# Performance work log

Hardware: AMD Instinct MI355X
Metric: run time of the kernel (lower is better)

The kernel has to match this reference:

```python
import jax, jax.numpy as jnp
import numpy as np

N_NODES = 49
FEAT_DIM = 1280            # efficientnet_v2_s feature dim
NODE_DIM = FEAT_DIM // N_NODES  # 26
GAT_HID = 256
HEADS = 4
NUM_CLASSES = 5
BATCH = 8192


def _grid_edges():
    # 7x7 grid, 8-neighborhood, as in _create_grid_edges, plus PyG default self loops
    edges = []
    for i in range(7):
        for j in range(7):
            node = i * 7 + j
            for di in (-1, 0, 1):
                for dj in (-1, 0, 1):
                    if di == 0 and dj == 0:
                        continue
                    ni, nj = i + di, j + dj
                    if 0 <= ni < 7 and 0 <= nj < 7:
                        edges.append((node, ni * 7 + nj))
    edges += [(n, n) for n in range(N_NODES)]  # add_self_loops=True (PyG default)
    return np.asarray(edges, dtype=np.int64).T  # [2, 361]


def setup_inputs() -> dict:
    key = jax.random.key(0)
    ks = jax.random.split(key, 16)
    s = 0.05
    inp = {
        "x": jax.random.normal(ks[0], (BATCH, FEAT_DIM), jnp.float32),
        "transform_w": jax.random.normal(ks[1], (FEAT_DIM, N_NODES * NODE_DIM), jnp.float32) * s,
        "transform_b": jnp.zeros((N_NODES * NODE_DIM,), jnp.float32),
        # GATv2 layer 1: 26 -> 64 per head, 4 heads, concat -> 256
        "g1_wl": jax.random.normal(ks[2], (NODE_DIM, GAT_HID), jnp.float32) * s,
        "g1_wr": jax.random.normal(ks[3], (NODE_DIM, GAT_HID), jnp.float32) * s,
        "g1_att": jax.random.normal(ks[4], (HEADS, GAT_HID // HEADS), jnp.float32) * s,
        "g1_b": jnp.zeros((GAT_HID,), jnp.float32),
        # GATv2 layer 2: 256 -> 256, 1 head, mean
        "g2_wl": jax.random.normal(ks[5], (GAT_HID, GAT_HID), jnp.float32) * s,
        "g2_wr": jax.random.normal(ks[6], (GAT_HID, GAT_HID), jnp.float32) * s,
        "g2_att": jax.random.normal(ks[7], (1, GAT_HID), jnp.float32) * s,
        "g2_b": jnp.zeros((GAT_HID,), jnp.float32),
        "fc_w": jax.random.normal(ks[8], (NODE_DIM + GAT_HID, NUM_CLASSES), jnp.float32) * s,
        "fc_b": jnp.zeros((NUM_CLASSES,), jnp.float32),
        "edge_index": jnp.asarray(_grid_edges()),
    }
    return inp


def _gatv2(x, src, dst, wl, wr, att, b, heads, out_ch, concat):
    # PyG GATv2Conv (share_weights=False, negative_slope=0.2, eval mode)
    n = x.shape[0]
    xl = (x @ wl).reshape(n, heads, out_ch)  # source messages
    xr = (x @ wr).reshape(n, heads, out_ch)  # target side of attention
    e = jax.nn.leaky_relu(xl[src] + xr[dst], 0.2)        # [E, H, C]
    score = jnp.einsum('ehc,hc->eh', e, att)             # [E, H]
    smax = jax.ops.segment_max(score, dst, num_segments=n)
    ex = jnp.exp(score - smax[dst])
    den = jax.ops.segment_sum(ex, dst, num_segments=n)
    alpha = ex / den[dst]                                # softmax over in-edges per node
    out = jax.ops.segment_sum(xl[src] * alpha[..., None], dst, num_segments=n)  # [N,H,C]
    out = out.reshape(n, heads * out_ch) if concat else out.mean(axis=1)
    return out + b


def reference(x, transform_w, transform_b, g1_wl, g1_wr, g1_att, g1_b,
              g2_wl, g2_wr, g2_att, g2_b, fc_w, fc_b, edge_index):
    src, dst = edge_index[0], edge_index[1]
    node = (x @ transform_w + transform_b).reshape(-1, N_NODES, NODE_DIM)  # [B,49,26]

    def graph(nf):
        h = _gatv2(nf, src, dst, g1_wl, g1_wr, g1_att, g1_b, HEADS, GAT_HID // HEADS, True)
        h = jax.nn.elu(h)  # dropout inactive in eval
        h = _gatv2(h, src, dst, g2_wl, g2_wr, g2_att, g2_b, 1, GAT_HID, False)
        return h  # [49, 256]

    g = jax.vmap(graph)(node)                              # [B,49,256]
    pooled = jnp.concatenate([node, g], axis=-1).mean(axis=1)  # [B, 282]
    return pooled @ fc_w + fc_b
```

## Files before the change

kernel.cpp:

```cpp
#include <hip/hip_runtime.h>
#include <hip/hip_bf16.h>

typedef __bf16 bf16;
typedef __attribute__((ext_vector_type(8))) __bf16 bf16x8;
typedef __attribute__((ext_vector_type(4))) __bf16 bf16x4;
typedef __attribute__((ext_vector_type(4))) float f32x4;

constexpr int BATCH = 8192, NN = 49, ND = 26, NOUT = 1274, FD = 1280;
constexpr int HID = 256, NE = 361, HEADS = 4;
constexpr int KT_X = 40;
constexpr int MT_X = 512;
constexpr int NB_W = 10;
constexpr int NTB  = 9;

constexpr size_t OFF_XPACK = 0;
constexpr size_t SZ_XPACK  = (size_t)MT_X * KT_X * 512 * 2;
constexpr size_t OFF_WPACK = OFF_XPACK + SZ_XPACK;
constexpr size_t SZ_WPACK  = (size_t)NB_W * NTB * KT_X * 512 * 2;
constexpr size_t OFF_B1    = OFF_WPACK + SZ_WPACK;
constexpr size_t SZ_B1     = (size_t)32 * 512 * 2;
constexpr size_t OFF_B2    = OFF_B1 + SZ_B1;
constexpr size_t SZ_B2     = (size_t)32 * 8 * 512 * 2;
constexpr size_t OFF_N32   = OFF_B2 + SZ_B2;
constexpr size_t SZ_N32    = (size_t)BATCH * NN * 32 * 2;
constexpr size_t OFF_PN    = OFF_N32 + SZ_N32;
constexpr size_t SZ_PN     = (size_t)BATCH * ND * 4;
constexpr size_t OFF_CSR   = OFF_PN + SZ_PN;
constexpr size_t SZ_CSR    = 8192;
constexpr size_t OFF_CHUNK = OFF_CSR + SZ_CSR;


__global__ __launch_bounds__(256) void k_pack_x(const float* __restrict__ x,
                                                bf16* __restrict__ xp) {
    int g = blockIdx.x * 256 + threadIdx.x;
    int lane = g & 63, frag = g >> 6;
    int mt = frag / KT_X, kt = frag - mt * KT_X;
    int row = mt * 16 + (lane & 15);
    int k0  = kt * 32 + (lane >> 4) * 8;
    const float* src = x + (size_t)row * FD + k0;
    bf16x8 v;
#pragma unroll
    for (int j = 0; j < 8; ++j) v[j] = (bf16)src[j];
    *(bf16x8*)(xp + ((size_t)frag * 64 + lane) * 8) = v;
}

__global__ __launch_bounds__(256) void k_pack_w(const float* __restrict__ w,
                                                bf16* __restrict__ wp) {
    int g = blockIdx.x * 256 + threadIdx.x;
    int lane = g & 63, frag = g >> 6;
    int kt = frag % KT_X, t2 = frag / KT_X;
    int nt = t2 % NTB, nb = t2 / NTB;
    int col = nb * 130 + nt * 16 + (lane & 15);
    int k0  = kt * 32 + (lane >> 4) * 8;
    bool ok = (col < NOUT) && (col < nb * 130 + 130);
    bf16x8 v;
#pragma unroll
    for (int j = 0; j < 8; ++j)
        v[j] = ok ? (bf16)w[(size_t)(k0 + j) * NOUT + col] : (bf16)0.f;
    *(bf16x8*)(wp + ((size_t)frag * 64 + lane) * 8) = v;
}

__global__ __launch_bounds__(256) void k_pack_g1(const float* __restrict__ wl,
                                                 const float* __restrict__ wr,
                                                 bf16* __restrict__ bp) {
    int g = blockIdx.x * 256 + threadIdx.x;
    int lane = g & 63, nt = g >> 6;
    int n  = nt * 16 + (lane & 15);
    int k0 = (lane >> 4) * 8;
    bf16x8 v;
#pragma unroll
    for (int j = 0; j < 8; ++j) {
        int k = k0 + j;
        float f = 0.f;
        if (k < ND) f = (n < HID) ? wl[k * HID + n] : wr[k * HID + (n - HID)];
        v[j] = (bf16)f;
    }
    *(bf16x8*)(bp + ((size_t)nt * 64 + lane) * 8) = v;
}

__global__ __launch_bounds__(256) void k_pack_g2(const float* __restrict__ wl,
                                                 const float* __restrict__ wr,
                                                 bf16* __restrict__ bp) {
    int g = blockIdx.x * 256 + threadIdx.x;
    int lane = g & 63, frag = g >> 6;
    int nt = frag >> 3, kt = frag & 7;
    int n  = nt * 16 + (lane & 15);
    int k0 = kt * 32 + (lane >> 4) * 8;
    bf16x8 v;
#pragma unroll
    for (int j = 0; j < 8; ++j) {
        int k = k0 + j;
        float f = (n < HID) ? wl[k * HID + n] : wr[k * HID + (n - HID)];
        v[j] = (bf16)f;
    }
    *(bf16x8*)(bp + ((size_t)frag * 64 + lane) * 8) = v;
}

__global__ __launch_bounds__(128) void k_csr_par(const int* __restrict__ ei,
                                                 int* __restrict__ csr) {
    __shared__ int es[NE], ed[NE], cnt[NN], ocnt[NN], off[NN + 1], ooff[NN + 1];
    int tid = threadIdx.x;
    if (tid < NN) { cnt[tid] = 0; ocnt[tid] = 0; }
    for (int e = tid; e < NE; e += 128) { es[e] = ei[e]; ed[e] = ei[NE + e]; }
    __syncthreads();
    for (int e = tid; e < NE; e += 128) {
        atomicAdd(&cnt[ed[e]], 1);
        atomicAdd(&ocnt[es[e]], 1);
    }
    __syncthreads();
    if (tid == 0) {
        off[0] = 0; ooff[0] = 0;
        for (int n = 0; n < NN; ++n) {
            off[n + 1] = off[n] + cnt[n];
            ooff[n + 1] = ooff[n] + ocnt[n];
        }
    }
    __syncthreads();
    if (tid < NN) {
        int p = off[tid];
        for (int e = 0; e < NE; ++e)
            if (ed[e] == tid) { csr[50 + p] = e; csr[411 + p] = es[e]; ++p; }
    } else if (tid >= 64 && tid < 64 + NN) {
        int n = tid - 64;
        int p = ooff[n];
        for (int e = 0; e < NE; ++e)
            if (es[e] == n) { csr[822 + p] = e; ++p; }
    }
    if (tid < 50) { csr[tid] = off[tid]; csr[772 + tid] = ooff[tid]; }
}

__global__ __launch_bounds__(256, 2) void k_gemm_node(const bf16* __restrict__ xp,
                                                      const bf16* __restrict__ wp,
                                                      const float* __restrict__ tb,
                                                      bf16* __restrict__ node32) {
    __shared__ bf16 L[128][148];
    __shared__ float tbS[144];
    int tid = threadIdx.x, lane = tid & 63, w = tid >> 6;
    int nb = blockIdx.y, C0 = nb * 130;
    int mt0 = blockIdx.x * 16 + w * 4;
    if (tid < 144) { int col = C0 + tid; tbS[tid] = (col < NOUT) ? tb[col] : 0.f; }
    f32x4 acc[4][9] = {};
    const bf16* wpB = wp + (size_t)(nb * NTB) * KT_X * 512;
    for (int kt = 0; kt < KT_X; ++kt) {
        bf16x8 a[4];
#pragma unroll
        for (int i = 0; i < 4; ++i)
            a[i] = *(const bf16x8*)(xp + (((size_t)(mt0 + i) * KT_X + kt) * 64 + lane) * 8);
#pragma unroll
        for (int j = 0; j < NTB; ++j) {
            bf16x8 b = *(const bf16x8*)(wpB + ((size_t)(j * KT_X + kt) * 64 + lane) * 8);
#pragma unroll
            for (int i = 0; i < 4; ++i)
                acc[i][j] = __builtin_amdgcn_mfma_f32_16x16x32_bf16(a[i], b, acc[i][j], 0, 0, 0);
        }
    }
    int c0 = lane & 15, r0 = (lane >> 4) * 4;
    int nodes = (nb == 9) ? 4 : 5;
    int total = 128 * nodes * 4;
    for (int half = 0; half < 2; ++half) {
        __syncthreads();
        if ((w >> 1) == half) {
            int lrbase = (w & 1) * 64;
#pragma unroll
            for (int i = 0; i < 4; ++i) {
#pragma unroll
                for (int j = 0; j < NTB; ++j) {
                    int col = j * 16 + c0;
                    float bias = tbS[col];
#pragma unroll
                    for (int r = 0; r < 4; ++r)
                        L[lrbase + i * 16 + r0 + r][col] = (bf16)(acc[i][j][r] + bias);
                }
            }
        }
        __syncthreads();
        int B0 = blockIdx.x * 256 + half * 128;
        for (int t = tid; t < total; t += 256) {
            int q = t & 3, t2 = t >> 2;
            int n_l = t2 % nodes, brow = t2 / nodes;
            bf16x8 o;
#pragma unroll
            for (int jj = 0; jj < 8; ++jj) {
                int d = q * 8 + jj;
                o[jj] = (d < ND) ? L[brow][n_l * 26 + d] : (bf16)0.f;
            }
            *(bf16x8*)(node32 + (((size_t)(B0 + brow) * NN + nb * 5 + n_l) * 32 + q * 8)) = o;
        }
    }
}

__global__ __launch_bounds__(256) void k_pool(const bf16* __restrict__ node32,
                                              float* __restrict__ pN) {
    int b = blockIdx.x * 8 + (threadIdx.x >> 5);
    int d = threadIdx.x & 31;
    if (d >= ND) return;
    const bf16* base = node32 + (size_t)b * NN * 32 + d;
    float s = 0.f;
    for (int n = 0; n < NN; ++n) s += (float)base[n * 32];
    pN[b * ND + d] = s;
}

__global__ __launch_bounds__(512, 2) void k_fuse1(const bf16* __restrict__ n32,
                                                  const bf16* __restrict__ B1p,
                                                  bf16* __restrict__ h1f,
                                                  const float* __restrict__ att1,
                                                  const float* __restrict__ g1b,
                                                  const int* __restrict__ ei,
                                                  const int* __restrict__ csr) {
    __shared__ __align__(16) char X[NN * 1024];
    __shared__ __align__(16) float attS[256];
    __shared__ float sc[NE * 4], srden[NN * 4], bS[256];
    __shared__ int ieOff[50], ieId[NE], ieSrc[NE], srcS[NE], dstS[NE];

    int tid = threadIdx.x, lane = tid & 63, w = tid >> 6, g = blockIdx.x;

    for (int i = tid; i < 256; i += 512) { attS[i] = att1[i]; bS[i] = g1b[i]; }
    for (int i = tid; i < NE; i += 512) {
        srcS[i] = ei[i]; dstS[i] = ei[NE + i];
        ieId[i] = csr[50 + i]; ieSrc[i] = csr[411 + i];
    }
    if (tid < 50) ieOff[tid] = csr[tid];

    {
        int mt = w & 3, ng = w >> 2;
        int m = mt * 16 + (lane & 15);
        bf16x8 bfrag = {};
        if (m < NN)
            bfrag = *(const bf16x8*)(n32 + ((size_t)(g * NN + m) * 32 + (lane >> 4) * 8));
        int chq = (lane >> 4) * 4;
        int sw = (m & 7) << 4;
        char* rowp = X + m * 1024;
#pragma unroll
        for (int j = 0; j < 16; ++j) {
            f32x4 z = {0.f, 0.f, 0.f, 0.f};
            bf16x8 afrag = *(const bf16x8*)(B1p + ((size_t)(ng * 16 + j) * 64 + lane) * 8);
            f32x4 acc = __builtin_amdgcn_mfma_f32_16x16x32_bf16(afrag, bfrag, z, 0, 0, 0);
            if (m < NN) {
                int ch = (ng * 16 + j) * 16 + chq;
                bf16x4 o4;
#pragma unroll
                for (int r = 0; r < 4; ++r) o4[r] = (bf16)acc[r];
                *(bf16x4*)(rowp + ((ch * 2) ^ sw)) = o4;
            }
        }
    }
    __syncthreads();

    int rot = tid & 7;
    for (int task = tid; task < NE * 4; task += 512) {
        int h = task / NE, e = task - h * NE;
        int s = srcS[e], d = dstS[e];
        int sws = (s & 7) << 4, swd = (d & 7) << 4;
        const char* ps = X + s * 1024;
        const char* pd = X + d * 1024;
        float pa[4] = {0.f, 0.f, 0.f, 0.f};
#pragma unroll
        for (int i = 0; i < 8; ++i) {
            int cc = ((i + rot) & 7) * 8;
            bf16x8 xl = *(const bf16x8*)(ps + (((h * 64 + cc) * 2) ^ sws));
            bf16x8 xr = *(const bf16x8*)(pd + (((256 + h * 64 + cc) * 2) ^ swd));
            float4 a0 = *(const float4*)(attS + h * 64 + cc);
            float4 a1 = *(const float4*)(attS + h * 64 + cc + 4);
            const float aa[8] = {a0.x, a0.y, a0.z, a0.w, a1.x, a1.y, a1.z, a1.w};
#pragma unroll
            for (int q = 0; q < 8; ++q) {
                float v = (float)xl[q] + (float)xr[q];
                v = v > 0.f ? v : 0.2f * v;
                pa[q & 3] = fmaf(aa[q], v, pa[q & 3]);
            }
        }
        sc[e * 4 + h] = (pa[0] + pa[1]) + (pa[2] + pa[3]);
    }
    __syncthreads();
    for (int t = tid; t < NN * 4; t += 512) {
        int n = t >> 2, h = t & 3;
        float m = -1e30f;
        for (int j = ieOff[n]; j < ieOff[n + 1]; ++j) m = fmaxf(m, sc[ieId[j] * 4 + h]);
        float den = 0.f;
        for (int j = ieOff[n]; j < ieOff[n + 1]; ++j) {
            int idx = ieId[j] * 4 + h;
            float ex = __expf(sc[idx] - m);
            sc[idx] = ex; den += ex;
        }
        srden[t] = 1.f / den;
    }
    __syncthreads();
    for (int task = tid; task < NN * 32; task += 512) {
        int n = task >> 5, cb = task & 31;
        int ch0 = cb * 8, hh = cb >> 3;
        float a8[8] = {};
        int j0 = ieOff[n], j1 = ieOff[n + 1];
        for (int j = j0; j < j1; ++j) {
            float al = sc[ieId[j] * 4 + hh];
            int s = ieSrc[j];
            bf16x8 xv = *(const bf16x8*)(X + s * 1024 + ((ch0 * 2) ^ ((s & 7) << 4)));
#pragma unroll
            for (int q = 0; q < 8; ++q) a8[q] = fmaf(al, (float)xv[q], a8[q]);
        }
        float rs = srden[n * 4 + hh];
        bf16x8 o;
#pragma unroll
        for (int q = 0; q < 8; ++q) {
            float v = fmaf(a8[q], rs, bS[ch0 + q]);
            v = v > 0.f ? v : (__expf(v) - 1.f);
            o[q] = (bf16)v;
        }
        int Rl = g * NN + n;
        int kt = ch0 >> 5, kg = (ch0 >> 3) & 3;
        size_t addr = (((size_t)(Rl >> 4) * 8 + kt) * 64 + (Rl & 15) + 16 * kg) * 8;
        *(bf16x8*)(h1f + addr) = o;
    }
}

__global__ __launch_bounds__(256) void k_gemm_l2(const bf16* __restrict__ Af,
                                                 const bf16* __restrict__ Bf,
                                                 bf16* __restrict__ xlr) {
    __shared__ bf16 LT[128][136];
    int tid = threadIdx.x, lane = tid & 63, w = tid >> 6;
    int mtb = blockIdx.x * 8 + (w >> 1) * 4;
    int ntb = blockIdx.y * 8 + (w & 1) * 4;
    f32x4 acc[4][4] = {};
    for (int kt = 0; kt < 8; ++kt) {
        bf16x8 a[4], b[4];
#pragma unroll
        for (int i = 0; i < 4; ++i)
            a[i] = *(const bf16x8*)(Af + (((size_t)(mtb + i) * 8 + kt) * 64 + lane) * 8);
#pragma unroll
        for (int j = 0; j < 4; ++j)
            b[j] = *(const bf16x8*)(Bf + (((size_t)(ntb + j) * 8 + kt) * 64 + lane) * 8);
#pragma unroll
        for (int i = 0; i < 4; ++i)
#pragma unroll
            for (int j = 0; j < 4; ++j)
                acc[i][j] = __builtin_amdgcn_mfma_f32_16x16x32_bf16(a[i], b[j], acc[i][j], 0, 0, 0);
    }
    int c0 = lane & 15, r0 = (lane >> 4) * 4;
    int lr0 = (w >> 1) * 64, lc0 = (w & 1) * 64;
#pragma unroll
    for (int i = 0; i < 4; ++i)
#pragma unroll
        for (int j = 0; j < 4; ++j)
#pragma unroll
            for (int r = 0; r < 4; ++r)
                LT[lr0 + i * 16 + r0 + r][lc0 + j * 16 + c0] = (bf16)acc[i][j][r];
    __syncthreads();
    size_t R0 = (size_t)blockIdx.x * 128, C0 = (size_t)blockIdx.y * 128;
#pragma unroll
    for (int it = 0; it < 8; ++it) {
        int idx = (it * 256 + tid) * 8;
        int r = idx >> 7, c = idx & 127;
        bf16x8 v = *(const bf16x8*)&LT[r][c];
        *(bf16x8*)(xlr + (R0 + r) * 512 + C0 + c) = v;
    }
}

static __device__ __forceinline__ float waveReduceSum(float v) {
#pragma unroll
    for (int m = 32; m > 0; m >>= 1) v += __shfl_xor(v, m, 64);
    return v;
}

__global__ __launch_bounds__(384, 2) void k_post2(const bf16* __restrict__ xlr,
                                                  const float* __restrict__ att2,
                                                  const float* __restrict__ pN,
                                                  const float* __restrict__ g2b,
                                                  const float* __restrict__ fcw,
                                                  const float* __restrict__ fcb,
                                                  const int* __restrict__ ei,
                                                  const int* __restrict__ csr,
                                                  int graph_base,
                                                  float* __restrict__ out) {
    __shared__ __align__(16) char X[NN * 1024];
    __shared__ float attS[256];
    __shared__ float sc[NE], sm[NN], sr[NN], wS[NN];
    __shared__ float poolS[288];
    int tid = threadIdx.x, g = blockIdx.x;
    const char* srcp = (const char*)(xlr + (size_t)g * NN * 512);
    for (int off = tid * 16; off < NN * 1024; off += 384 * 16) {
        int row = off >> 10;
        *(uint4*)(X + (off ^ ((row & 7) << 4))) = *(const uint4*)(srcp + off);
    }
    if (tid < 256) attS[tid] = att2[tid];
    if (tid >= 256 && tid < 256 + ND)
        poolS[tid - 256] = pN[(size_t)(graph_base + g) * ND + (tid - 256)] * (1.f / NN);
    __syncthreads();
    if (tid < NE) {
        int s = ei[tid], d = ei[NE + tid];
        int sws = (s & 7) << 4, swd = (d & 7) << 4;
        const char* ps = X + s * 1024;
        const char* pd = X + d * 1024;
        int rot = tid & 7;
        float pa[4] = {0.f, 0.f, 0.f, 0.f};
#pragma unroll 8
        for (int i = 0; i < 32; ++i) {
            int cc = ((i + rot) & 31) * 8;
            bf16x8 xl = *(const bf16x8*)(ps + ((cc * 2) ^ sws));
            bf16x8 xr = *(const bf16x8*)(pd + (((256 + cc) * 2) ^ swd));
            float4 a0 = *(const float4*)(attS + cc);
            float4 a1 = *(const float4*)(attS + cc + 4);
            const float aa[8] = {a0.x, a0.y, a0.z, a0.w, a1.x, a1.y, a1.z, a1.w};
#pragma unroll
            for (int q = 0; q < 8; ++q) {
                float v = (float)xl[q] + (float)xr[q];
                v = v > 0.f ? v : 0.2f * v;
                pa[q & 3] = fmaf(aa[q], v, pa[q & 3]);
            }
        }
        sc[tid] = (pa[0] + pa[1]) + (pa[2] + pa[3]);
    }
    __syncthreads();
    if (tid < NN) {
        int j0 = csr[tid], j1 = csr[tid + 1];
        float m = -1e30f;
        for (int j = j0; j < j1; ++j) m = fmaxf(m, sc[csr[50 + j]]);
        float den = 0.f;
        for (int j = j0; j < j1; ++j) den += __expf(sc[csr[50 + j]] - m);
        sm[tid] = m; sr[tid] = 1.f / den;
    }
    __syncthreads();
    if (tid < NN) {
        float wa = 0.f;
        int j0 = csr[772 + tid], j1 = csr[772 + tid + 1];
        for (int j = j0; j < j1; ++j) {
            int e = csr[822 + j];
            int d = ei[NE + e];
            wa += __expf(sc[e] - sm[d]) * sr[d];
        }
        wS[tid] = wa;
    }
    __syncthreads();
    if (tid < HID) {
        float acc = 0.f;
#pragma unroll
        for (int n = 0; n < NN; ++n) {
            float v = (float)*(const bf16*)(X + n * 1024 + ((tid * 2) ^ ((n & 7) << 4)));
            acc = fmaf(wS[n], v, acc);
        }
        poolS[ND + tid] = acc * (1.f / NN) + g2b[tid];
    }
    __syncthreads();
    int w5 = tid >> 6, lane = tid & 63;
    if (w5 < 5) {
        float a = 0.f;
        for (int d = lane; d < ND + HID; d += 64) a = fmaf(poolS[d], fcw[d * 5 + w5], a);
        a = waveReduceSum(a);
        if (lane == 0) out[(size_t)(graph_base + g) * 5 + w5] = a + fcb[w5];
    }
}

extern "C" void kernel_launch(void* const* d_in, const int* in_sizes, int n_in,
                              void* d_out, int out_size, void* d_ws, size_t ws_size,
                              hipStream_t stream) {
    const float* x   = (const float*)d_in[0];
    const float* tw  = (const float*)d_in[1];
    const float* tb  = (const float*)d_in[2];
    const float* wl1 = (const float*)d_in[3];
    const float* wr1 = (const float*)d_in[4];
    const float* at1 = (const float*)d_in[5];
    const float* b1  = (const float*)d_in[6];
    const float* wl2 = (const float*)d_in[7];
    const float* wr2 = (const float*)d_in[8];
    const float* at2 = (const float*)d_in[9];
    const float* b2  = (const float*)d_in[10];
    const float* fcw = (const float*)d_in[11];
    const float* fcb = (const float*)d_in[12];
    const int*   ei  = (const int*)d_in[13];
    float* out = (float*)d_out;

    char* ws = (char*)d_ws;
    bf16*  xp   = (bf16*)(ws + OFF_XPACK);
    bf16*  wp   = (bf16*)(ws + OFF_WPACK);
    bf16*  b1p  = (bf16*)(ws + OFF_B1);
    bf16*  b2p  = (bf16*)(ws + OFF_B2);
    bf16*  n32  = (bf16*)(ws + OFF_N32);
    float* pN   = (float*)(ws + OFF_PN);
    int*   csr  = (int*)(ws + OFF_CSR);

    const size_t perC = 50176 + 12544;
    int C = 512;
    for (int cand : {2048, 1024, 512}) {
        if (OFF_CHUNK + (size_t)cand * perC <= ws_size) { C = cand; break; }
    }
    bf16*  xlr = (bf16*)(ws + OFF_CHUNK);
    bf16*  h1f = (bf16*)(ws + OFF_CHUNK + (size_t)C * 50176);
    int nchunks = BATCH / C;
    int MtC = C * NN / 16;

    k_pack_x<<<dim3(MT_X * KT_X * 64 / 256), dim3(256), 0, stream>>>(x, xp);
    k_pack_w<<<dim3(NB_W * NTB * KT_X * 64 / 256), dim3(256), 0, stream>>>(tw, wp);
    k_pack_g1<<<dim3(8), dim3(256), 0, stream>>>(wl1, wr1, b1p);
    k_pack_g2<<<dim3(64), dim3(256), 0, stream>>>(wl2, wr2, b2p);
    k_csr_par<<<dim3(1), dim3(128), 0, stream>>>(ei, csr);
    k_gemm_node<<<dim3(32, NB_W), dim3(256), 0, stream>>>(xp, wp, tb, n32);
    k_pool<<<dim3(BATCH / 8), dim3(256), 0, stream>>>(n32, pN);

    for (int c = 0; c < nchunks; ++c) {
        const bf16* n32c = n32 + (size_t)c * C * NN * 32;
        k_fuse1<<<dim3(C), dim3(512), 0, stream>>>(n32c, b1p, h1f, at1, b1, ei, csr);
        k_gemm_l2<<<dim3(MtC / 8, 4), dim3(256), 0, stream>>>(h1f, b2p, xlr);
        k_post2<<<dim3(C), dim3(384), 0, stream>>>(xlr, at2, pN, b2, fcw, fcb,
                                                   ei, csr, c * C, out);
    }
}
```

Baseline: 959.2 us.

## Fuse layer-2 GEMM into per-graph attention kernel, dropping xlr round trip

Removes the separate layer-2 GEMM kernel and computes each graph's xl/xr projection inside the post-processing kernel with MFMA, writing results straight into swizzled shared memory. h1f is repacked per graph (padded to 64 rows) so each block reads its own A tiles, which eliminates the global xlr buffer write and reread and one launch per chunk. In exchange, each block rereads the full 256x512 B matrix from cache, pads 49 rows to 64, and holds 128 accumulator vectors per thread, which raises register pressure and may lower occupancy.

New measurement: 962.6 us. About the same (+0.3%).

```diff
diff --git a/kernel.cpp b/kernel.cpp
--- a/kernel.cpp
+++ b/kernel.cpp
@@ -305,52 +305,9 @@
             v = v > 0.f ? v : (__expf(v) - 1.f);
             o[q] = (bf16)v;
         }
-        int Rl = g * NN + n;
         int kt = ch0 >> 5, kg = (ch0 >> 3) & 3;
-        size_t addr = (((size_t)(Rl >> 4) * 8 + kt) * 64 + (Rl & 15) + 16 * kg) * 8;
+        size_t addr = ((((size_t)g * 4 + (n >> 4)) * 8 + kt) * 64 + (n & 15) + 16 * kg) * 8;
         *(bf16x8*)(h1f + addr) = o;
-    }
-}
-
-__global__ __launch_bounds__(256) void k_gemm_l2(const bf16* __restrict__ Af,
-                                                 const bf16* __restrict__ Bf,
-                                                 bf16* __restrict__ xlr) {
-    __shared__ bf16 LT[128][136];
-    int tid = threadIdx.x, lane = tid & 63, w = tid >> 6;
-    int mtb = blockIdx.x * 8 + (w >> 1) * 4;
-    int ntb = blockIdx.y * 8 + (w & 1) * 4;
-    f32x4 acc[4][4] = {};
-    for (int kt = 0; kt < 8; ++kt) {
-        bf16x8 a[4], b[4];
-#pragma unroll
-        for (int i = 0; i < 4; ++i)
-            a[i] = *(const bf16x8*)(Af + (((size_t)(mtb + i) * 8 + kt) * 64 + lane) * 8);
-#pragma unroll
-        for (int j = 0; j < 4; ++j)
-            b[j] = *(const bf16x8*)(Bf + (((size_t)(ntb + j) * 8 + kt) * 64 + lane) * 8);
-#pragma unroll
-        for (int i = 0; i < 4; ++i)
-#pragma unroll
-            for (int j = 0; j < 4; ++j)
-                acc[i][j] = __builtin_amdgcn_mfma_f32_16x16x32_bf16(a[i], b[j], acc[i][j], 0, 0, 0);
-    }
-    int c0 = lane & 15, r0 = (lane >> 4) * 4;
-    int lr0 = (w >> 1) * 64, lc0 = (w & 1) * 64;
-#pragma unroll
-    for (int i = 0; i < 4; ++i)
-#pragma unroll
-        for (int j = 0; j < 4; ++j)
-#pragma unroll
-            for (int r = 0; r < 4; ++r)
-                LT[lr0 + i * 16 + r0 + r][lc0 + j * 16 + c0] = (bf16)acc[i][j][r];
-    __syncthreads();
-    size_t R0 = (size_t)blockIdx.x * 128, C0 = (size_t)blockIdx.y * 128;
-#pragma unroll
-    for (int it = 0; it < 8; ++it) {
-        int idx = (it * 256 + tid) * 8;
-        int r = idx >> 7, c = idx & 127;
-        bf16x8 v = *(const bf16x8*)&LT[r][c];
-        *(bf16x8*)(xlr + (R0 + r) * 512 + C0 + c) = v;
     }
 }
 
@@ -360,7 +317,8 @@
     return v;
 }
 
-__global__ __launch_bounds__(384, 2) void k_post2(const bf16* __restrict__ xlr,
+__global__ __launch_bounds__(256, 2) void k_fuse2(const bf16* __restrict__ h1f,
+                                                  const bf16* __restrict__ B2p,
                                                   const float* __restrict__ att2,
                                                   const float* __restrict__ pN,
                                                   const float* __restrict__ g2b,
@@ -374,22 +332,55 @@
     __shared__ float attS[256];
     __shared__ float sc[NE], sm[NN], sr[NN], wS[NN];
     __shared__ float poolS[288];
-    int tid = threadIdx.x, g = blockIdx.x;
-    const char* srcp = (const char*)(xlr + (size_t)g * NN * 512);
-    for (int off = tid * 16; off < NN * 1024; off += 384 * 16) {
-        int row = off >> 10;
-        *(uint4*)(X + (off ^ ((row & 7) << 4))) = *(const uint4*)(srcp + off);
-    }
+    int tid = threadIdx.x, lane = tid & 63, w = tid >> 6, g = blockIdx.x;
+
     if (tid < 256) attS[tid] = att2[tid];
-    if (tid >= 256 && tid < 256 + ND)
-        poolS[tid - 256] = pN[(size_t)(graph_base + g) * ND + (tid - 256)] * (1.f / NN);
-    __syncthreads();
-    if (tid < NE) {
-        int s = ei[tid], d = ei[NE + tid];
+    if (tid < ND) poolS[tid] = pN[(size_t)(graph_base + g) * ND + tid] * (1.f / NN);
+
+    {
+        int mtp = w & 1, chf = w >> 1;
+        f32x4 acc0[16] = {};
+        f32x4 acc1[16] = {};
+        const bf16* aBase0 = h1f + (((size_t)g * 4 + mtp * 2 + 0) * 8) * 512;
+        const bf16* aBase1 = h1f + (((size_t)g * 4 + mtp * 2 + 1) * 8) * 512;
+        for (int kt = 0; kt < 8; ++kt) {
+            bf16x8 a0 = *(const bf16x8*)(aBase0 + ((size_t)kt * 64 + lane) * 8);
+            bf16x8 a1 = *(const bf16x8*)(aBase1 + ((size_t)kt * 64 + lane) * 8);
+#pragma unroll
+            for (int j = 0; j < 16; ++j) {
+                int nt = chf * 16 + j;
+                bf16x8 b = *(const bf16x8*)(B2p + (((size_t)nt * 8 + kt) * 64 + lane) * 8);
+                acc0[j] = __builtin_amdgcn_mfma_f32_16x16x32_bf16(b, a0, acc0[j], 0, 0, 0);
+                acc1[j] = __builtin_amdgcn_mfma_f32_16x16x32_bf16(b, a1, acc1[j], 0, 0, 0);
+            }
+        }
+        int chq = (lane >> 4) * 4;
+#pragma unroll
+        for (int i = 0; i < 2; ++i) {
+            int n = (mtp * 2 + i) * 16 + (lane & 15);
+            if (n < NN) {
+                int sw = (n & 7) << 4;
+                char* rowp = X + n * 1024;
+#pragma unroll
+                for (int j = 0; j < 16; ++j) {
+                    int ch = (chf * 16 + j) * 16 + chq;
+                    f32x4 acc = i ? acc1[j] : acc0[j];
+                    bf16x4 o4;
+#pragma unroll
+                    for (int r = 0; r < 4; ++r) o4[r] = (bf16)acc[r];
+                    *(bf16x4*)(rowp + ((ch * 2) ^ sw)) = o4;
+                }
+            }
+        }
+    }
+    __syncthreads();
+
+    for (int e = tid; e < NE; e += 256) {
+        int s = ei[e], d = ei[NE + e];
         int sws = (s & 7) << 4, swd = (d & 7) << 4;
         const char* ps = X + s * 1024;
         const char* pd = X + d * 1024;
-        int rot = tid & 7;
+        int rot = e & 7;
         float pa[4] = {0.f, 0.f, 0.f, 0.f};
 #pragma unroll 8
         for (int i = 0; i < 32; ++i) {
@@ -406,7 +397,7 @@
                 pa[q & 3] = fmaf(aa[q], v, pa[q & 3]);
             }
         }
-        sc[tid] = (pa[0] + pa[1]) + (pa[2] + pa[3]);
+        sc[e] = (pa[0] + pa[1]) + (pa[2] + pa[3]);
     }
     __syncthreads();
     if (tid < NN) {
@@ -429,7 +420,7 @@
         wS[tid] = wa;
     }
     __syncthreads();
-    if (tid < HID) {
+    {
         float acc = 0.f;
 #pragma unroll
         for (int n = 0; n < NN; ++n) {
@@ -439,12 +430,11 @@
         poolS[ND + tid] = acc * (1.f / NN) + g2b[tid];
     }
     __syncthreads();
-    int w5 = tid >> 6, lane = tid & 63;
-    if (w5 < 5) {
+    for (int o = w; o < 5; o += 4) {
         float a = 0.f;
-        for (int d = lane; d < ND + HID; d += 64) a = fmaf(poolS[d], fcw[d * 5 + w5], a);
+        for (int d = lane; d < ND + HID; d += 64) a = fmaf(poolS[d], fcw[d * 5 + o], a);
         a = waveReduceSum(a);
-        if (lane == 0) out[(size_t)(graph_base + g) * 5 + w5] = a + fcb[w5];
+        if (lane == 0) out[(size_t)(graph_base + g) * 5 + o] = a + fcb[o];
     }
 }
 
@@ -476,15 +466,13 @@
     float* pN   = (float*)(ws + OFF_PN);
     int*   csr  = (int*)(ws + OFF_CSR);
 
-    const size_t perC = 50176 + 12544;
+    const size_t perC = 32768;
     int C = 512;
     for (int cand : {2048, 1024, 512}) {
         if (OFF_CHUNK + (size_t)cand * perC <= ws_size) { C = cand; break; }
     }
-    bf16*  xlr = (bf16*)(ws + OFF_CHUNK);
-    bf16*  h1f = (bf16*)(ws + OFF_CHUNK + (size_t)C * 50176);
+    bf16* h1f = (bf16*)(ws + OFF_CHUNK);
     int nchunks = BATCH / C;
-    int MtC = C * NN / 16;
 
     k_pack_x<<<dim3(MT_X * KT_X * 64 / 256), dim3(256), 0, stream>>>(x, xp);
     k_pack_w<<<dim3(NB_W * NTB * KT_X * 64 / 256), dim3(256), 0, stream>>>(tw, wp);
@@ -497,8 +485,7 @@
     for (int c = 0; c < nchunks; ++c) {
         const bf16* n32c = n32 + (size_t)c * C * NN * 32;
         k_fuse1<<<dim3(C), dim3(512), 0, stream>>>(n32c, b1p, h1f, at1, b1, ei, csr);
-        k_gemm_l2<<<dim3(MtC / 8, 4), dim3(256), 0, stream>>>(h1f, b2p, xlr);
-        k_post2<<<dim3(C), dim3(384), 0, stream>>>(xlr, at2, pN, b2, fcw, fcb,
+        k_fuse2<<<dim3(C), dim3(256), 0, stream>>>(h1f, b2p, at2, pN, b2, fcw, fcb,
                                                    ei, csr, c * C, out);
     }
 }
```
